# Performance work log

Hardware: AMD Instinct MI355X
Metric: run time of the kernel (lower is better)

The kernel has to match this reference:

```python
import jax, jax.numpy as jnp
import numpy as np

B, S, I, H, O = 128, 1024, 256, 512, 256
N_TARGETS = 1


def setup_inputs() -> dict:
    key = jax.random.key(0)
    k0, k1, k2, k3, k4 = jax.random.split(key, 5)
    s_ih = 1.0 / np.sqrt(I + H)   # PyTorch Linear default init bound
    s_ho = 1.0 / np.sqrt(H)
    return {
        "sequences": jax.random.normal(k0, (B, S, I), dtype=jnp.float32),
        "W_i2h": jax.random.uniform(k1, (H, I + H), jnp.float32, -s_ih, s_ih),
        "b_i2h": jax.random.uniform(k2, (H,), jnp.float32, -s_ih, s_ih),
        "W_h2o": jax.random.uniform(k3, (O, H), jnp.float32, -s_ho, s_ho),
        "b_h2o": jax.random.uniform(k4, (O,), jnp.float32, -s_ho, s_ho),
    }


def reference(sequences, W_i2h, b_i2h, W_h2o, b_h2o):
    # Elman RNN: h_t = tanh(W_i2h @ [x_t; h_{t-1}] + b); output from last
    # N_TARGETS steps via h2o. cat+linear == x@Wx + h@Wh (split columns).
    b, seq_len, in_dim = sequences.shape
    hid = W_i2h.shape[0]
    Wx = W_i2h[:, :in_dim].T   # (I, H)
    Wh = W_i2h[:, in_dim:].T   # (H, H)
    h0 = jnp.zeros((b, hid), dtype=sequences.dtype)
    xs = jnp.transpose(sequences, (1, 0, 2))  # (S, B, I) for scan over time

    def step(h, x):
        h = jnp.tanh(x @ Wx + h @ Wh + b_i2h)
        return h, None

    # first S - n_targets steps: state updates only
    h, _ = jax.lax.scan(step, h0, xs[: seq_len - N_TARGETS])

    def step_out(h, x):
        h = jnp.tanh(x @ Wx + h @ Wh + b_i2h)
        o = h @ W_h2o.T + b_h2o
        return h, o

    # last n_targets steps: state update + output projection
    hidden, outs = jax.lax.scan(step_out, h, xs[seq_len - N_TARGETS:])
    output = jnp.transpose(outs, (1, 0, 2))  # (B, n_targets, O)
    return output, hidden
```

## Files before the change

kernel.cpp:

```cpp
#include <hip/hip_runtime.h>

typedef _Float16 h2f __attribute__((ext_vector_type(2)));
typedef _Float16 f16x8 __attribute__((ext_vector_type(8)));
typedef float f32x4 __attribute__((ext_vector_type(4)));
typedef unsigned int u32;
typedef unsigned short u16;

#define B_ 128
#define S_ 1024
#define I_ 256
#define H_ 512
#define O_ 256
#define IH_ 768

#if __has_builtin(__builtin_amdgcn_fdot2)
__device__ __forceinline__ float fdot2u(u32 a, u32 b, float c) {
    return __builtin_amdgcn_fdot2(__builtin_bit_cast(h2f, a),
                                  __builtin_bit_cast(h2f, b), c, false);
}
#else
__device__ __forceinline__ float fdot2u(u32 a, u32 b, float c) {
    h2f av = __builtin_bit_cast(h2f, a), bv = __builtin_bit_cast(h2f, b);
    return c + (float)av.x * (float)bv.x + (float)av.y * (float)bv.y;
}
#endif

__device__ __forceinline__ u32 pack2(float x, float y) {
    return __builtin_bit_cast(u32, __builtin_amdgcn_cvt_pkrtz(x, y));
}
__device__ __forceinline__ u16 f2h(float x) { return __builtin_bit_cast(u16, (_Float16)x); }
__device__ __forceinline__ float h2f_(u16 x) { return (float)__builtin_bit_cast(_Float16, x); }

__device__ __forceinline__ float tanh_fast(float x) {
    float e = __expf(-2.f * fabsf(x));
    float r = (1.f - e) / (1.f + e);
    return copysignf(r, x);
}

__device__ __forceinline__ f32x4 mfx(uint4 a, uint4 b, f32x4 c) {
    return __builtin_amdgcn_mfma_f32_16x16x32_f16(
        __builtin_bit_cast(f16x8, a), __builtin_bit_cast(f16x8, b), c, 0, 0, 0);
}
__device__ __forceinline__ f32x4 mf(uint4 a, const uint4* bp, f32x4 c) {
    uint4 b = *bp;
    return mfx(a, b, c);
}

#define REP8(X)  X(0) X(1) X(2) X(3) X(4) X(5) X(6) X(7)
#define REP16(X) REP8(X) X(8) X(9) X(10) X(11) X(12) X(13) X(14) X(15)
#define REPK10(X) X(0) X(1) X(2) X(3) X(4) X(5) X(6) X(7) X(8) X(9)

#define WXB_OFF 0
#define WHB_OFF (256u << 10)
#define PRE_OFF (1u << 20)

__global__ __launch_bounds__(256) void k_convert(const float* __restrict__ W,
                                                 uint4* __restrict__ wxb4,
                                                 uint4* __restrict__ whb4) {
    int idx = blockIdx.x * 256 + threadIdx.x;
    if (idx < 16384) {
        int q = idx >> 9, col = idx & 511;
        const float4* r = (const float4*)(W + (long)col * IH_ + q * 8);
        float4 u = r[0], v = r[1];
        wxb4[idx] = (uint4){pack2(u.x, u.y), pack2(u.z, u.w),
                            pack2(v.x, v.y), pack2(v.z, v.w)};
    } else {
        int i2 = idx - 16384;
        int q = i2 >> 9, n = i2 & 511;
        const float4* r = (const float4*)(W + (long)n * IH_ + I_ + q * 8);
        float4 u = r[0], v = r[1];
        whb4[i2] = (uint4){pack2(u.x, u.y), pack2(u.z, u.w),
                           pack2(v.x, v.y), pack2(v.z, v.w)};
    }
}

__global__ __launch_bounds__(256) __attribute__((amdgpu_waves_per_eu(2, 2)))
void k_phase1(const float* __restrict__ seq, const uint4* __restrict__ wxb4,
              const float* __restrict__ bias, u16* __restrict__ pre) {
    int w = threadIdx.x >> 6, l = threadIdx.x & 63;
    int lm = l & 15, lq = l >> 4;
    int mb_w = blockIdx.x * 64 + w * 16;
    long xrow = (long)(mb_w + lm) * I_;
#define DECLA1(k) uint4 a##k; { \
        const float4* xp = (const float4*)(seq + xrow + (k)*32 + lq*8); \
        float4 u = xp[0], v = xp[1]; \
        a##k = (uint4){pack2(u.x,u.y), pack2(u.z,u.w), pack2(v.x,v.y), pack2(v.z,v.w)}; }
    REP8(DECLA1)
#undef DECLA1
    int mrow0 = mb_w + lq * 4;
#pragma unroll
    for (int half = 0; half < 2; ++half) {
        int colbase = half * 256;
        const uint4* bptr = wxb4 + colbase + lm;
#define DECLC(n) float bv##n = bias[colbase + (n)*16 + lm]; \
                 f32x4 c##n = {bv##n, bv##n, bv##n, bv##n};
        REP16(DECLC)
#undef DECLC
#define ROW(k,n) c##n = mf(a##k, bptr + ((k)*4 + lq)*512 + (n)*16, c##n);
#define KS(k) ROW(k,0) ROW(k,1) ROW(k,2) ROW(k,3) ROW(k,4) ROW(k,5) ROW(k,6) ROW(k,7) \
              ROW(k,8) ROW(k,9) ROW(k,10) ROW(k,11) ROW(k,12) ROW(k,13) ROW(k,14) ROW(k,15)
        KS(0) KS(1) KS(2) KS(3) KS(4) KS(5) KS(6) KS(7)
#undef KS
#undef ROW
#define STN(n) { long cb = (long)colbase + (n)*16 + lm; \
        pre[(long)(mrow0+0)*H_ + cb] = f2h(c##n[0]); \
        pre[(long)(mrow0+1)*H_ + cb] = f2h(c##n[1]); \
        pre[(long)(mrow0+2)*H_ + cb] = f2h(c##n[2]); \
        pre[(long)(mrow0+3)*H_ + cb] = f2h(c##n[3]); }
        REP16(STN)
#undef STN
    }
}

__global__ __launch_bounds__(512) __attribute__((amdgpu_waves_per_eu(2, 2)))
void k_phase2(const u16* __restrict__ pre, const uint4* __restrict__ whb4,
              const float* __restrict__ Who, const float* __restrict__ bo,
              float* __restrict__ out) {
    __shared__ __align__(16) uint4 wlds[16 * 512];
    __shared__ __align__(16) u16 hbuf[2][H_];
    int b = blockIdx.x, j = threadIdx.x;
    int w = j >> 6, lane = j & 63;
    int n_ = lane & 15, gq = lane >> 4;
    int colbase = w * 64;
    int cb0 = colbase, cb1 = colbase + 16, cb2 = colbase + 32, cb3 = colbase + 48;
#define DECLB(K) \
    uint4 b##K##_0 = whb4[(4*(K) + gq) * 512 + cb0 + n_]; \
    uint4 b##K##_1 = whb4[(4*(K) + gq) * 512 + cb1 + n_]; \
    uint4 b##K##_2 = whb4[(4*(K) + gq) * 512 + cb2 + n_]; \
    uint4 b##K##_3 = whb4[(4*(K) + gq) * 512 + cb3 + n_];
    REPK10(DECLB)
#undef DECLB
#pragma unroll
    for (int s_ = 0; s_ < 16; ++s_) wlds[s_ * 512 + j] = whb4[(40 + s_) * 512 + j];
    const u16* pr = pre + (long)b * S_ * H_ + colbase + n_;
    hbuf[0][j] = 0;
    __syncthreads();
    u16 pv0 = pr[0], pv1 = pr[16], pv2 = pr[32], pv3 = pr[48];
    for (int t = 0; t < S_; ++t) {
        int cur = t & 1, nxt = cur ^ 1;
        long tn = (t + 1 < S_) ? (long)(t + 1) : (long)t;
        int zoff = 0, lz = 0;
        asm volatile("" : "+v"(zoff), "+v"(lz));
#define SLOADK(K, P) \
        uint4 s##P##_0 = whb4[(4*(K) + gq) * 512 + cb0 + n_ + zoff]; \
        uint4 s##P##_1 = whb4[(4*(K) + gq) * 512 + cb1 + n_ + zoff]; \
        uint4 s##P##_2 = whb4[(4*(K) + gq) * 512 + cb2 + n_ + zoff]; \
        uint4 s##P##_3 = whb4[(4*(K) + gq) * 512 + cb3 + n_ + zoff];
        SLOADK(14, e)
        SLOADK(15, f)
#undef SLOADK
        u16 pn0 = pr[tn * H_ +  0];
        u16 pn1 = pr[tn * H_ + 16];
        u16 pn2 = pr[tn * H_ + 32];
        u16 pn3 = pr[tn * H_ + 48];
        const u16* hc = hbuf[cur];
#define DECLA(K) uint4 a##K = *(const uint4*)(hc + 32*(K) + 8*gq);
#define LB(K) \
        uint4 l##K##_0 = wlds[(4*((K)-10) + gq) * 512 + cb0 + n_ + lz]; \
        uint4 l##K##_1 = wlds[(4*((K)-10) + gq) * 512 + cb1 + n_ + lz]; \
        uint4 l##K##_2 = wlds[(4*((K)-10) + gq) * 512 + cb2 + n_ + lz]; \
        uint4 l##K##_3 = wlds[(4*((K)-10) + gq) * 512 + cb3 + n_ + lz];
#define MK4(K, B0, B1, B2, B3) \
        c0 = mfx(a##K, B0, c0); c1 = mfx(a##K, B1, c1); \
        c2 = mfx(a##K, B2, c2); c3 = mfx(a##K, B3, c3);
        float p0f = h2f_(pv0), p1f = h2f_(pv1), p2f = h2f_(pv2), p3f = h2f_(pv3);
        f32x4 c0 = {p0f, p0f, p0f, p0f};
        f32x4 c1 = {p1f, p1f, p1f, p1f};
        f32x4 c2 = {p2f, p2f, p2f, p2f};
        f32x4 c3 = {p3f, p3f, p3f, p3f};
        DECLA(0) DECLA(1) DECLA(2) DECLA(3)
        MK4(0, b0_0, b0_1, b0_2, b0_3)
        MK4(1, b1_0, b1_1, b1_2, b1_3)
        MK4(2, b2_0, b2_1, b2_2, b2_3)
        DECLA(4) DECLA(5) DECLA(6) DECLA(7)
        MK4(3, b3_0, b3_1, b3_2, b3_3)
        MK4(4, b4_0, b4_1, b4_2, b4_3)
        MK4(5, b5_0, b5_1, b5_2, b5_3)
        LB(10) LB(11)
        DECLA(8) DECLA(9) DECLA(10) DECLA(11)
        MK4(6, b6_0, b6_1, b6_2, b6_3)
        MK4(7, b7_0, b7_1, b7_2, b7_3)
        MK4(8, b8_0, b8_1, b8_2, b8_3)
        LB(12) LB(13)
        DECLA(12) DECLA(13) DECLA(14) DECLA(15)
        MK4(9, b9_0, b9_1, b9_2, b9_3)
        MK4(10, l10_0, l10_1, l10_2, l10_3)
        MK4(11, l11_0, l11_1, l11_2, l11_3)
        MK4(12, l12_0, l12_1, l12_2, l12_3)
        MK4(13, l13_0, l13_1, l13_2, l13_3)
        MK4(14, se_0, se_1, se_2, se_3)
        MK4(15, sf_0, sf_1, sf_2, sf_3)
#undef MK4
#undef LB
#undef DECLA
        float v = c0[0];
        v = (gq == 1) ? c1[0] : v;
        v = (gq == 2) ? c2[0] : v;
        v = (gq == 3) ? c3[0] : v;
        hbuf[nxt][colbase + lane] = f2h(tanh_fast(v));
        pv0 = pn0; pv1 = pn1; pv2 = pn2; pv3 = pn3;
        __syncthreads();
    }
    float hj = h2f_(hbuf[0][j]);
    out[(long)B_ * O_ + (long)b * H_ + j] = hj;
    if (j < O_) {
        float acc = bo[j];
        const float4* wr = (const float4*)(Who + (long)j * H_);
        const u16* hb = hbuf[0];
#pragma unroll 4
        for (int k = 0; k < 128; ++k) {
            float4 wv = wr[k];
            acc += h2f_(hb[4 * k + 0]) * wv.x
                 + h2f_(hb[4 * k + 1]) * wv.y
                 + h2f_(hb[4 * k + 2]) * wv.z
                 + h2f_(hb[4 * k + 3]) * wv.w;
        }
        out[(long)b * O_ + j] = acc;
    }
}

__global__ __launch_bounds__(512) void k_fallback(const float* __restrict__ seq,
                                                  const float* __restrict__ W,
                                                  const float* __restrict__ bias,
                                                  const float* __restrict__ Who,
                                                  const float* __restrict__ bo,
                                                  float* __restrict__ out) {
    __shared__ float hb[2][H_];
    int b = blockIdx.x, j = threadIdx.x;
    const float* wrow = W + (long)j * IH_;
    float bj = bias[j];
    hb[0][j] = 0.f;
    __syncthreads();
    for (int t = 0; t < S_; ++t) {
        const float* x = seq + ((long)b * S_ + t) * I_;
        float acc = bj;
        for (int i = 0; i < I_; ++i) acc += x[i] * wrow[i];
        const float* hc = hb[t & 1];
        for (int k = 0; k < H_; ++k) acc += hc[k] * wrow[I_ + k];
        hb[(t & 1) ^ 1][j] = tanh_fast(acc);
        __syncthreads();
    }
    float hj = hb[0][j];
    out[(long)B_ * O_ + (long)b * H_ + j] = hj;
    if (j < O_) {
        float acc = bo[j];
        const float* wr = Who + (long)j * H_;
        for (int k = 0; k < H_; ++k) acc += hb[0][k] * wr[k];
        out[(long)b * O_ + j] = acc;
    }
}

extern "C" void kernel_launch(void* const* d_in, const int* in_sizes, int n_in,
                              void* d_out, int out_size, void* d_ws, size_t ws_size,
                              hipStream_t stream) {
    const float* seq = (const float*)d_in[0];
    const float* W   = (const float*)d_in[1];
    const float* bi  = (const float*)d_in[2];
    const float* Who = (const float*)d_in[3];
    const float* bo  = (const float*)d_in[4];
    float* out = (float*)d_out;

    const size_t WS_NEED = (size_t)PRE_OFF + (size_t)B_ * S_ * H_ * 2;

    if (ws_size >= WS_NEED) {
        char* ws = (char*)d_ws;
        uint4* wxb4 = (uint4*)(ws + WXB_OFF);
        uint4* whb4 = (uint4*)(ws + WHB_OFF);
        u16*   pre  = (u16*)(ws + PRE_OFF);
        k_convert<<<192, 256, 0, stream>>>(W, wxb4, whb4);
        k_phase1<<<2048, 256, 0, stream>>>(seq, wxb4, bi, pre);
        k_phase2<<<B_, 512, 0, stream>>>(pre, whb4, Who, bo, out);
    } else {
        k_fallback<<<B_, 512, 0, stream>>>(seq, W, bi, Who, bo, out);
    }
}
```

Before: 1.941 ms.

## Halve phase2 block to 4 waves, each computing 128 hidden columns

The recurrent kernel now runs 256 threads per batch row instead of 512, so each wave owns 128 output columns with 8 accumulator tiles. 11 K-slices of Wh stay in registers, 3 come from LDS and 2 are streamed from global memory each step, with one of those global loads moved into the middle of the MFMA chain. Fewer waves means cheaper per-step barriers and better reuse of the A fragment across MFMAs, at the cost of higher register pressure (waves_per_eu 1) and less latency hiding per step.

Result: slower. 4.076 ms (+110.0%).

```diff
diff --git a/kernel.cpp b/kernel.cpp
--- a/kernel.cpp
+++ b/kernel.cpp
@@ -48,7 +48,7 @@
 
 #define REP8(X)  X(0) X(1) X(2) X(3) X(4) X(5) X(6) X(7)
 #define REP16(X) REP8(X) X(8) X(9) X(10) X(11) X(12) X(13) X(14) X(15)
-#define REPK10(X) X(0) X(1) X(2) X(3) X(4) X(5) X(6) X(7) X(8) X(9)
+#define REPK11(X) X(0) X(1) X(2) X(3) X(4) X(5) X(6) X(7) X(8) X(9) X(10)
 
 #define WXB_OFF 0
 #define WHB_OFF (256u << 10)
@@ -112,100 +112,151 @@
     }
 }
 
-__global__ __launch_bounds__(512) __attribute__((amdgpu_waves_per_eu(2, 2)))
+__global__ __launch_bounds__(256) __attribute__((amdgpu_waves_per_eu(1, 1)))
 void k_phase2(const u16* __restrict__ pre, const uint4* __restrict__ whb4,
               const float* __restrict__ Who, const float* __restrict__ bo,
               float* __restrict__ out) {
-    __shared__ __align__(16) uint4 wlds[16 * 512];
+    __shared__ __align__(16) uint4 wlds[12 * 512];
     __shared__ __align__(16) u16 hbuf[2][H_];
-    int b = blockIdx.x, j = threadIdx.x;
-    int w = j >> 6, lane = j & 63;
+    int b = blockIdx.x, t_ = threadIdx.x;
+    int w = t_ >> 6, lane = t_ & 63;
     int n_ = lane & 15, gq = lane >> 4;
-    int colbase = w * 64;
-    int cb0 = colbase, cb1 = colbase + 16, cb2 = colbase + 32, cb3 = colbase + 48;
+    int colbase = w * 128;
+    int cb0 = colbase,      cb1 = colbase + 16,  cb2 = colbase + 32,  cb3 = colbase + 48;
+    int cb4 = colbase + 64, cb5 = colbase + 80,  cb6 = colbase + 96,  cb7 = colbase + 112;
 #define DECLB(K) \
     uint4 b##K##_0 = whb4[(4*(K) + gq) * 512 + cb0 + n_]; \
     uint4 b##K##_1 = whb4[(4*(K) + gq) * 512 + cb1 + n_]; \
     uint4 b##K##_2 = whb4[(4*(K) + gq) * 512 + cb2 + n_]; \
-    uint4 b##K##_3 = whb4[(4*(K) + gq) * 512 + cb3 + n_];
-    REPK10(DECLB)
+    uint4 b##K##_3 = whb4[(4*(K) + gq) * 512 + cb3 + n_]; \
+    uint4 b##K##_4 = whb4[(4*(K) + gq) * 512 + cb4 + n_]; \
+    uint4 b##K##_5 = whb4[(4*(K) + gq) * 512 + cb5 + n_]; \
+    uint4 b##K##_6 = whb4[(4*(K) + gq) * 512 + cb6 + n_]; \
+    uint4 b##K##_7 = whb4[(4*(K) + gq) * 512 + cb7 + n_];
+    REPK11(DECLB)
 #undef DECLB
 #pragma unroll
-    for (int s_ = 0; s_ < 16; ++s_) wlds[s_ * 512 + j] = whb4[(40 + s_) * 512 + j];
+    for (int s_ = 0; s_ < 24; ++s_) wlds[s_ * 256 + t_] = whb4[44 * 512 + s_ * 256 + t_];
     const u16* pr = pre + (long)b * S_ * H_ + colbase + n_;
-    hbuf[0][j] = 0;
+    hbuf[0][t_] = 0;
+    hbuf[0][t_ + 256] = 0;
     __syncthreads();
-    u16 pv0 = pr[0], pv1 = pr[16], pv2 = pr[32], pv3 = pr[48];
+    u16 pv0 = pr[0],  pv1 = pr[16], pv2 = pr[32],  pv3 = pr[48];
+    u16 pv4 = pr[64], pv5 = pr[80], pv6 = pr[96],  pv7 = pr[112];
     for (int t = 0; t < S_; ++t) {
         int cur = t & 1, nxt = cur ^ 1;
         long tn = (t + 1 < S_) ? (long)(t + 1) : (long)t;
         int zoff = 0, lz = 0;
         asm volatile("" : "+v"(zoff), "+v"(lz));
-#define SLOADK(K, P) \
-        uint4 s##P##_0 = whb4[(4*(K) + gq) * 512 + cb0 + n_ + zoff]; \
-        uint4 s##P##_1 = whb4[(4*(K) + gq) * 512 + cb1 + n_ + zoff]; \
-        uint4 s##P##_2 = whb4[(4*(K) + gq) * 512 + cb2 + n_ + zoff]; \
-        uint4 s##P##_3 = whb4[(4*(K) + gq) * 512 + cb3 + n_ + zoff];
-        SLOADK(14, e)
-        SLOADK(15, f)
-#undef SLOADK
-        u16 pn0 = pr[tn * H_ +  0];
-        u16 pn1 = pr[tn * H_ + 16];
-        u16 pn2 = pr[tn * H_ + 32];
-        u16 pn3 = pr[tn * H_ + 48];
+#define SLOADK(K) \
+        uint4 s##K##_0 = whb4[(4*(K) + gq) * 512 + cb0 + n_ + zoff]; \
+        uint4 s##K##_1 = whb4[(4*(K) + gq) * 512 + cb1 + n_ + zoff]; \
+        uint4 s##K##_2 = whb4[(4*(K) + gq) * 512 + cb2 + n_ + zoff]; \
+        uint4 s##K##_3 = whb4[(4*(K) + gq) * 512 + cb3 + n_ + zoff]; \
+        uint4 s##K##_4 = whb4[(4*(K) + gq) * 512 + cb4 + n_ + zoff]; \
+        uint4 s##K##_5 = whb4[(4*(K) + gq) * 512 + cb5 + n_ + zoff]; \
+        uint4 s##K##_6 = whb4[(4*(K) + gq) * 512 + cb6 + n_ + zoff]; \
+        uint4 s##K##_7 = whb4[(4*(K) + gq) * 512 + cb7 + n_ + zoff];
+        SLOADK(14)
+        u16 pn0 = pr[tn * H_ +  0], pn1 = pr[tn * H_ + 16];
+        u16 pn2 = pr[tn * H_ + 32], pn3 = pr[tn * H_ + 48];
+        u16 pn4 = pr[tn * H_ + 64], pn5 = pr[tn * H_ + 80];
+        u16 pn6 = pr[tn * H_ + 96], pn7 = pr[tn * H_ + 112];
         const u16* hc = hbuf[cur];
 #define DECLA(K) uint4 a##K = *(const uint4*)(hc + 32*(K) + 8*gq);
 #define LB(K) \
-        uint4 l##K##_0 = wlds[(4*((K)-10) + gq) * 512 + cb0 + n_ + lz]; \
-        uint4 l##K##_1 = wlds[(4*((K)-10) + gq) * 512 + cb1 + n_ + lz]; \
-        uint4 l##K##_2 = wlds[(4*((K)-10) + gq) * 512 + cb2 + n_ + lz]; \
-        uint4 l##K##_3 = wlds[(4*((K)-10) + gq) * 512 + cb3 + n_ + lz];
-#define MK4(K, B0, B1, B2, B3) \
-        c0 = mfx(a##K, B0, c0); c1 = mfx(a##K, B1, c1); \
-        c2 = mfx(a##K, B2, c2); c3 = mfx(a##K, B3, c3);
+        uint4 l##K##_0 = wlds[(4*((K)-11) + gq) * 512 + cb0 + n_ + lz]; \
+        uint4 l##K##_1 = wlds[(4*((K)-11) + gq) * 512 + cb1 + n_ + lz]; \
+        uint4 l##K##_2 = wlds[(4*((K)-11) + gq) * 512 + cb2 + n_ + lz]; \
+        uint4 l##K##_3 = wlds[(4*((K)-11) + gq) * 512 + cb3 + n_ + lz]; \
+        uint4 l##K##_4 = wlds[(4*((K)-11) + gq) * 512 + cb4 + n_ + lz]; \
+        uint4 l##K##_5 = wlds[(4*((K)-11) + gq) * 512 + cb5 + n_ + lz]; \
+        uint4 l##K##_6 = wlds[(4*((K)-11) + gq) * 512 + cb6 + n_ + lz]; \
+        uint4 l##K##_7 = wlds[(4*((K)-11) + gq) * 512 + cb7 + n_ + lz];
+#define MK8R(K) \
+        c0 = mfx(a##K, b##K##_0, c0); c1 = mfx(a##K, b##K##_1, c1); \
+        c2 = mfx(a##K, b##K##_2, c2); c3 = mfx(a##K, b##K##_3, c3); \
+        c4 = mfx(a##K, b##K##_4, c4); c5 = mfx(a##K, b##K##_5, c5); \
+        c6 = mfx(a##K, b##K##_6, c6); c7 = mfx(a##K, b##K##_7, c7);
+#define MK8L(K) \
+        c0 = mfx(a##K, l##K##_0, c0); c1 = mfx(a##K, l##K##_1, c1); \
+        c2 = mfx(a##K, l##K##_2, c2); c3 = mfx(a##K, l##K##_3, c3); \
+        c4 = mfx(a##K, l##K##_4, c4); c5 = mfx(a##K, l##K##_5, c5); \
+        c6 = mfx(a##K, l##K##_6, c6); c7 = mfx(a##K, l##K##_7, c7);
+#define MK8S(K) \
+        c0 = mfx(a##K, s##K##_0, c0); c1 = mfx(a##K, s##K##_1, c1); \
+        c2 = mfx(a##K, s##K##_2, c2); c3 = mfx(a##K, s##K##_3, c3); \
+        c4 = mfx(a##K, s##K##_4, c4); c5 = mfx(a##K, s##K##_5, c5); \
+        c6 = mfx(a##K, s##K##_6, c6); c7 = mfx(a##K, s##K##_7, c7);
         float p0f = h2f_(pv0), p1f = h2f_(pv1), p2f = h2f_(pv2), p3f = h2f_(pv3);
+        float p4f = h2f_(pv4), p5f = h2f_(pv5), p6f = h2f_(pv6), p7f = h2f_(pv7);
         f32x4 c0 = {p0f, p0f, p0f, p0f};
         f32x4 c1 = {p1f, p1f, p1f, p1f};
         f32x4 c2 = {p2f, p2f, p2f, p2f};
         f32x4 c3 = {p3f, p3f, p3f, p3f};
-        DECLA(0) DECLA(1) DECLA(2) DECLA(3)
-        MK4(0, b0_0, b0_1, b0_2, b0_3)
-        MK4(1, b1_0, b1_1, b1_2, b1_3)
-        MK4(2, b2_0, b2_1, b2_2, b2_3)
-        DECLA(4) DECLA(5) DECLA(6) DECLA(7)
-        MK4(3, b3_0, b3_1, b3_2, b3_3)
-        MK4(4, b4_0, b4_1, b4_2, b4_3)
-        MK4(5, b5_0, b5_1, b5_2, b5_3)
-        LB(10) LB(11)
-        DECLA(8) DECLA(9) DECLA(10) DECLA(11)
-        MK4(6, b6_0, b6_1, b6_2, b6_3)
-        MK4(7, b7_0, b7_1, b7_2, b7_3)
-        MK4(8, b8_0, b8_1, b8_2, b8_3)
-        LB(12) LB(13)
-        DECLA(12) DECLA(13) DECLA(14) DECLA(15)
-        MK4(9, b9_0, b9_1, b9_2, b9_3)
-        MK4(10, l10_0, l10_1, l10_2, l10_3)
-        MK4(11, l11_0, l11_1, l11_2, l11_3)
-        MK4(12, l12_0, l12_1, l12_2, l12_3)
-        MK4(13, l13_0, l13_1, l13_2, l13_3)
-        MK4(14, se_0, se_1, se_2, se_3)
-        MK4(15, sf_0, sf_1, sf_2, sf_3)
-#undef MK4
+        f32x4 c4 = {p4f, p4f, p4f, p4f};
+        f32x4 c5 = {p5f, p5f, p5f, p5f};
+        f32x4 c6 = {p6f, p6f, p6f, p6f};
+        f32x4 c7 = {p7f, p7f, p7f, p7f};
+        DECLA(0) DECLA(1)
+        MK8R(0)
+        DECLA(2)
+        MK8R(1)
+        DECLA(3)
+        MK8R(2)
+        DECLA(4)
+        MK8R(3)
+        DECLA(5)
+        MK8R(4)
+        SLOADK(15)
+        DECLA(6)
+        MK8R(5)
+        DECLA(7)
+        MK8R(6)
+        LB(11)
+        DECLA(8)
+        MK8R(7)
+        DECLA(9)
+        MK8R(8)
+        LB(12)
+        DECLA(10)
+        MK8R(9)
+        DECLA(11)
+        MK8R(10)
+        LB(13)
+        DECLA(12) DECLA(13)
+        MK8L(11)
+        DECLA(14)
+        MK8L(12)
+        DECLA(15)
+        MK8L(13)
+        MK8S(14)
+        MK8S(15)
+#undef MK8R
+#undef MK8L
+#undef MK8S
 #undef LB
 #undef DECLA
-        float v = c0[0];
-        v = (gq == 1) ? c1[0] : v;
-        v = (gq == 2) ? c2[0] : v;
-        v = (gq == 3) ? c3[0] : v;
-        hbuf[nxt][colbase + lane] = f2h(tanh_fast(v));
+#undef SLOADK
+        float v0 = c0[0];
+        v0 = (gq == 1) ? c1[0] : v0;
+        v0 = (gq == 2) ? c2[0] : v0;
+        v0 = (gq == 3) ? c3[0] : v0;
+        float v1 = c4[0];
+        v1 = (gq == 1) ? c5[0] : v1;
+        v1 = (gq == 2) ? c6[0] : v1;
+        v1 = (gq == 3) ? c7[0] : v1;
+        hbuf[nxt][colbase + lane] = f2h(tanh_fast(v0));
+        hbuf[nxt][colbase + 64 + lane] = f2h(tanh_fast(v1));
         pv0 = pn0; pv1 = pn1; pv2 = pn2; pv3 = pn3;
+        pv4 = pn4; pv5 = pn5; pv6 = pn6; pv7 = pn7;
         __syncthreads();
     }
-    float hj = h2f_(hbuf[0][j]);
-    out[(long)B_ * O_ + (long)b * H_ + j] = hj;
-    if (j < O_) {
-        float acc = bo[j];
-        const float4* wr = (const float4*)(Who + (long)j * H_);
+    out[(long)B_ * O_ + (long)b * H_ + t_] = h2f_(hbuf[0][t_]);
+    out[(long)B_ * O_ + (long)b * H_ + t_ + 256] = h2f_(hbuf[0][t_ + 256]);
+    {
+        float acc = bo[t_];
+        const float4* wr = (const float4*)(Who + (long)t_ * H_);
         const u16* hb = hbuf[0];
 #pragma unroll 4
         for (int k = 0; k < 128; ++k) {
@@ -215,7 +266,7 @@
                  + h2f_(hb[4 * k + 2]) * wv.z
                  + h2f_(hb[4 * k + 3]) * wv.w;
         }
-        out[(long)b * O_ + j] = acc;
+        out[(long)b * O_ + t_] = acc;
     }
 }
 
@@ -269,7 +320,7 @@
         u16*   pre  = (u16*)(ws + PRE_OFF);
         k_convert<<<192, 256, 0, stream>>>(W, wxb4, whb4);
         k_phase1<<<2048, 256, 0, stream>>>(seq, wxb4, bi, pre);
-        k_phase2<<<B_, 512, 0, stream>>>(pre, whb4, Who, bo, out);
+        k_phase2<<<B_, 256, 0, stream>>>(pre, whb4, Who, bo, out);
     } else {
         k_fallback<<<B_, 512, 0, stream>>>(seq, W, bi, Who, bo, out);
     }
```
